# Kernel optimization log

Measured on AMD Instinct MI355X. Metric: run time of the kernel, lower is better.

The kernel has to match this reference:

```python
import jax, jax.numpy as jnp
import numpy as np

B, C_IN, H, W = 8, 64, 224, 224
C_OUT, HID = 64, 64
KH = KW = 3
IN_SZ = C_IN * KH * KW  # 576, unfold feature size (c, kh, kw order)


def setup_inputs() -> dict:
    key = jax.random.key(0)
    k_x, k_w1, k_b1, k_w2, k_b2 = jax.random.split(key, 5)
    bound1 = 1.0 / np.sqrt(IN_SZ)
    bound2 = 1.0 / np.sqrt(HID)
    return {
        "x": jax.random.normal(k_x, (B, C_IN, H, W), dtype=jnp.float32),
        "W1": jax.random.uniform(k_w1, (HID, IN_SZ), jnp.float32, -bound1, bound1),
        "b1": jax.random.uniform(k_b1, (HID,), jnp.float32, -bound1, bound1),
        "W2": jax.random.uniform(k_w2, (C_OUT, HID), jnp.float32, -bound2, bound2),
        "b2": jax.random.uniform(k_b2, (C_OUT,), jnp.float32, -bound2, bound2),
    }


def reference(x, W1, b1, W2, b2):
    # First Linear over unfold patches == implicit-GEMM conv: W1 rows are
    # flattened (c, kh, kw) exactly matching F.unfold's feature ordering.
    w_conv = W1.reshape(HID, C_IN, KH, KW)
    h = jax.lax.conv_general_dilated(
        x, w_conv,
        window_strides=(1, 1),
        padding=((1, 1), (1, 1)),
        rhs_dilation=(1, 1),
        dimension_numbers=("NCHW", "OIHW", "NCHW"),
    ) + b1[None, :, None, None]
    h = jax.nn.relu(h)
    # Second Linear acts per patch location == pointwise (1x1) contraction.
    out = jnp.einsum("bchw,oc->bohw", h, W2) + b2[None, :, None, None]
    return out
```

## Files before the change

### kernel.cpp

```cpp
#include <hip/hip_runtime.h>

typedef __attribute__((ext_vector_type(8))) short bf16x8;
typedef __attribute__((ext_vector_type(4))) float f32x4;

static constexpr int HH = 224, WW = 224;
static constexpr int CIN = 64;
static constexpr int HW = HH * WW;

__device__ __forceinline__ ushort f2bf(float f) {
    unsigned u = __builtin_bit_cast(unsigned, f);
    u += 0x7FFFu + ((u >> 16) & 1u);
    return (ushort)(u >> 16);
}

__global__ void prep_kernel(const float* __restrict__ W1, const float* __restrict__ W2,
                            ushort* __restrict__ ws, int nfill) {
    const int idx = blockIdx.x * 256 + threadIdx.x;
    if (idx < 36864) {
        const int ch = idx >> 12;
        const int n = (idx >> 6) & 63;
        const int c = idx & 63;
        ws[idx] = f2bf(W1[n * 576 + c * 9 + ch]);
    } else if (idx < 40960) {
        ws[idx] = f2bf(W2[idx - 36864]);
    } else if (idx < nfill) {
        ws[idx] = 0;
    }
}

__global__ __launch_bounds__(256)
void xprep_kernel(const float* __restrict__ xin, ushort* __restrict__ xt) {
    const int b = blockIdx.y;
    const float* xg = xin + (size_t)b * (CIN * HW);
    ushort* xo = xt + (size_t)b * ((size_t)HW * 64);
    const int base = blockIdx.x * 1024 + threadIdx.x;
    #pragma unroll
    for (int it = 0; it < 4; ++it) {
        const int idx = base + it * 256;
        const int p = ((idx >> 9) << 6) | (idx & 63);
        const int cg = (idx >> 6) & 7;
        bf16x8 o;
        #pragma unroll
        for (int j = 0; j < 8; ++j)
            o[j] = (short)f2bf(xg[(cg * 8 + j) * HW + p]);
        *reinterpret_cast<bf16x8*>(xo + (size_t)p * 64 + cg * 8) = o;
    }
}

#define GLD_LDS16(g, l) __builtin_amdgcn_global_load_lds(                  \
    (const __attribute__((address_space(1))) void*)(g),                    \
    (__attribute__((address_space(3))) void*)(l), 16, 0, 0)

__global__ __launch_bounds__(256, 3)
void mlpconv_fast(const ushort* __restrict__ xt, const ushort* __restrict__ w1r,
                  const float* __restrict__ b1, const ushort* __restrict__ w2r,
                  const float* __restrict__ b2, const ushort* __restrict__ zp,
                  float* __restrict__ out) {
    __shared__ ushort xs[10 * 40 * 64];

    const int tid = threadIdx.x;
    const int wave = tid >> 6;
    const int lane = tid & 63;
    const int l15 = lane & 15;
    const int quad = lane >> 4;

    const int x0 = blockIdx.x * 32;
    const int y0 = blockIdx.y * 8;
    const int b = blockIdx.z;

    const ushort* xtb = xt + (size_t)b * ((size_t)HW * 64);

    const int lpx = lane >> 3;
    const int laneoff = lpx * 64 + (((lane & 7) ^ lpx) * 8);

    for (int q = wave; q < 50; q += 4) {
        const int r = q / 5;
        const int i = q - 5 * r;
        const int gy = y0 + r - 1;
        const int gx0 = x0 - 4 + i * 8;
        const ushort* real = xtb + (long)(gy * WW + gx0) * 64 + laneoff;
        const bool ok = ((unsigned)gy < (unsigned)HH) &
                        ((unsigned)(gx0 + lpx) < (unsigned)WW);
        const ushort* src = ok ? real : zp;
        GLD_LDS16(src, &xs[(r * 40 + i * 8) * 64]);
    }

    float b1v[4];
    #pragma unroll
    for (int nt = 0; nt < 4; ++nt) b1v[nt] = b1[nt * 16 + l15];

    f32x4 acc[4][4];
    #pragma unroll
    for (int mt = 0; mt < 4; ++mt)
        #pragma unroll
        for (int nt = 0; nt < 4; ++nt)
            acc[mt][nt] = (f32x4){b1v[nt], b1v[nt], b1v[nt], b1v[nt]};

    asm volatile("s_waitcnt vmcnt(0)" ::: "memory");
    __syncthreads();

    #pragma unroll 2
    for (int ks = 0; ks < 18; ++ks) {
        const int ch = ks >> 1;
        const int s = ks & 1;
        const int dy = ch / 3, dx = ch - 3 * (ch / 3);
        const int ko = s * 32 + quad * 8;
        bf16x8 bfr[4];
        #pragma unroll
        for (int nt = 0; nt < 4; ++nt)
            bfr[nt] = *reinterpret_cast<const bf16x8*>(
                w1r + ch * 4096 + (nt * 16 + l15) * 64 + ko);
        const int kswz = ko ^ (((l15 + dx + 3) & 7) * 8);
        #pragma unroll
        for (int mt = 0; mt < 4; ++mt) {
            const int row = 2 * wave + (mt >> 1) + dy;
            const int col = (mt & 1) * 16 + l15 + dx + 3;
            const bf16x8 afr = *reinterpret_cast<const bf16x8*>(
                &xs[(row * 40 + col) * 64 + kswz]);
            #pragma unroll
            for (int nt = 0; nt < 4; ++nt)
                acc[mt][nt] = __builtin_amdgcn_mfma_f32_16x16x32_bf16(
                    afr, bfr[nt], acc[mt][nt], 0, 0, 0);
        }
    }

    __syncthreads();

    float4 b2q[4];
    #pragma unroll
    for (int it = 0; it < 4; ++it)
        b2q[it] = *reinterpret_cast<const float4*>(b2 + it * 16 + quad * 4);

    bf16x8 wa2[2][4];
    #pragma unroll
    for (int k2 = 0; k2 < 2; ++k2)
        #pragma unroll
        for (int it = 0; it < 4; ++it)
            wa2[k2][it] = *reinterpret_cast<const bf16x8*>(
                w2r + (it * 16 + l15) * 64 + k2 * 32 + quad * 8);

    ushort* myh = &xs[wave * (16 * 72)];
    float* outg = out + (size_t)b * (64 * HH * WW);

    #pragma unroll
    for (int mt = 0; mt < 4; ++mt) {
        #pragma unroll
        for (int ni = 0; ni < 4; ++ni)
            #pragma unroll
            for (int r = 0; r < 4; ++r) {
                float v = acc[mt][ni][r];
                v = v > 0.f ? v : 0.f;
                myh[(quad * 4 + r) * 72 + ni * 16 + l15] = f2bf(v);
            }
        f32x4 acc2[4];
        #pragma unroll
        for (int it = 0; it < 4; ++it)
            acc2[it] = (f32x4){b2q[it].x, b2q[it].y, b2q[it].z, b2q[it].w};
        #pragma unroll
        for (int k2 = 0; k2 < 2; ++k2) {
            const bf16x8 hb = *reinterpret_cast<const bf16x8*>(
                &myh[l15 * 72 + k2 * 32 + quad * 8]);
            #pragma unroll
            for (int it = 0; it < 4; ++it)
                acc2[it] = __builtin_amdgcn_mfma_f32_16x16x32_bf16(
                    wa2[k2][it], hb, acc2[it], 0, 0, 0);
        }
        const int gy = y0 + 2 * wave + (mt >> 1);
        const int gx = x0 + (mt & 1) * 16 + l15;
        #pragma unroll
        for (int it = 0; it < 4; ++it)
            #pragma unroll
            for (int r = 0; r < 4; ++r) {
                const int o = it * 16 + quad * 4 + r;
                outg[(o * HH + gy) * WW + gx] = acc2[it][r];
            }
    }
}

__global__ __launch_bounds__(256, 3)
void mlpconv_kernel(const float* __restrict__ xin, const ushort* __restrict__ w1r,
                    const float* __restrict__ b1, const ushort* __restrict__ w2r,
                    const float* __restrict__ b2, float* __restrict__ out) {
    __shared__ ushort xs[10 * 40 * 64];

    const int tid = threadIdx.x;
    const int wave = tid >> 6;
    const int lane = tid & 63;
    const int l15 = lane & 15;
    const int quad = lane >> 4;

    const int x0 = blockIdx.x * 32;
    const int y0 = blockIdx.y * 8;
    const int b = blockIdx.z;

    const float* xg = xin + (size_t)b * (CIN * HH * WW);

    for (int e = tid; e < 6400; e += 256) {
        const int i = e % 10;
        const int t = e / 10;
        const int c = t & 63;
        const int r = t >> 6;
        const int gy = y0 + r - 1;
        const int gx4 = x0 - 4 + i * 4;
        float4 v = make_float4(0.f, 0.f, 0.f, 0.f);
        if (((unsigned)gy < (unsigned)HH) && ((unsigned)gx4 <= 220u))
            v = *reinterpret_cast<const float4*>(xg + (c * HH + gy) * WW + gx4);
        const int p0 = r * 40 + i * 4;
        xs[(p0 + 0) * 64 + (c ^ (((p0 + 0) & 7) * 8))] = f2bf(v.x);
        xs[(p0 + 1) * 64 + (c ^ (((p0 + 1) & 7) * 8))] = f2bf(v.y);
        xs[(p0 + 2) * 64 + (c ^ (((p0 + 2) & 7) * 8))] = f2bf(v.z);
        xs[(p0 + 3) * 64 + (c ^ (((p0 + 3) & 7) * 8))] = f2bf(v.w);
    }

    float b1v[4];
    #pragma unroll
    for (int nt = 0; nt < 4; ++nt) b1v[nt] = b1[nt * 16 + l15];

    f32x4 acc[4][4];
    #pragma unroll
    for (int mt = 0; mt < 4; ++mt)
        #pragma unroll
        for (int nt = 0; nt < 4; ++nt)
            acc[mt][nt] = (f32x4){b1v[nt], b1v[nt], b1v[nt], b1v[nt]};

    __syncthreads();

    #pragma unroll 2
    for (int ks = 0; ks < 18; ++ks) {
        const int ch = ks >> 1;
        const int s = ks & 1;
        const int dy = ch / 3, dx = ch - 3 * (ch / 3);
        const int ko = s * 32 + quad * 8;
        bf16x8 bfr[4];
        #pragma unroll
        for (int nt = 0; nt < 4; ++nt)
            bfr[nt] = *reinterpret_cast<const bf16x8*>(
                w1r + ch * 4096 + (nt * 16 + l15) * 64 + ko);
        const int kswz = ko ^ (((l15 + dx + 3) & 7) * 8);
        #pragma unroll
        for (int mt = 0; mt < 4; ++mt) {
            const int row = 2 * wave + (mt >> 1) + dy;
            const int col = (mt & 1) * 16 + l15 + dx + 3;
            const bf16x8 afr = *reinterpret_cast<const bf16x8*>(
                &xs[(row * 40 + col) * 64 + kswz]);
            #pragma unroll
            for (int nt = 0; nt < 4; ++nt)
                acc[mt][nt] = __builtin_amdgcn_mfma_f32_16x16x32_bf16(
                    afr, bfr[nt], acc[mt][nt], 0, 0, 0);
        }
    }

    __syncthreads();

    float4 b2q[4];
    #pragma unroll
    for (int it = 0; it < 4; ++it)
        b2q[it] = *reinterpret_cast<const float4*>(b2 + it * 16 + quad * 4);

    bf16x8 wa2[2][4];
    #pragma unroll
    for (int k2 = 0; k2 < 2; ++k2)
        #pragma unroll
        for (int it = 0; it < 4; ++it)
            wa2[k2][it] = *reinterpret_cast<const bf16x8*>(
                w2r + (it * 16 + l15) * 64 + k2 * 32 + quad * 8);

    ushort* myh = &xs[wave * (16 * 72)];
    float* outg = out + (size_t)b * (64 * HH * WW);

    #pragma unroll
    for (int mt = 0; mt < 4; ++mt) {
        #pragma unroll
        for (int ni = 0; ni < 4; ++ni)
            #pragma unroll
            for (int r = 0; r < 4; ++r) {
                float v = acc[mt][ni][r];
                v = v > 0.f ? v : 0.f;
                myh[(quad * 4 + r) * 72 + ni * 16 + l15] = f2bf(v);
            }
        f32x4 acc2[4];
        #pragma unroll
        for (int it = 0; it < 4; ++it)
            acc2[it] = (f32x4){b2q[it].x, b2q[it].y, b2q[it].z, b2q[it].w};
        #pragma unroll
        for (int k2 = 0; k2 < 2; ++k2) {
            const bf16x8 hb = *reinterpret_cast<const bf16x8*>(
                &myh[l15 * 72 + k2 * 32 + quad * 8]);
            #pragma unroll
            for (int it = 0; it < 4; ++it)
                acc2[it] = __builtin_amdgcn_mfma_f32_16x16x32_bf16(
                    wa2[k2][it], hb, acc2[it], 0, 0, 0);
        }
        const int gy = y0 + 2 * wave + (mt >> 1);
        const int gx = x0 + (mt & 1) * 16 + l15;
        #pragma unroll
        for (int it = 0; it < 4; ++it)
            #pragma unroll
            for (int r = 0; r < 4; ++r) {
                const int o = it * 16 + quad * 4 + r;
                outg[(o * HH + gy) * WW + gx] = acc2[it][r];
            }
    }
}

extern "C" void kernel_launch(void* const* d_in, const int* in_sizes, int n_in,
                              void* d_out, int out_size, void* d_ws, size_t ws_size,
                              hipStream_t stream) {
    const float* x  = (const float*)d_in[0];
    const float* W1 = (const float*)d_in[1];
    const float* b1 = (const float*)d_in[2];
    const float* W2 = (const float*)d_in[3];
    const float* b2 = (const float*)d_in[4];
    float* out = (float*)d_out;

    ushort* ws  = (ushort*)d_ws;
    ushort* w1r = ws;
    ushort* w2r = ws + 36864;
    ushort* zp  = ws + 40960;
    ushort* xt  = ws + 41024;

    const size_t need = (size_t)41024 * 2 + (size_t)8 * HW * 64 * 2;
    const bool fast = ws_size >= need;

    prep_kernel<<<161, 256, 0, stream>>>(W1, W2, ws, fast ? 41024 : 40960);
    dim3 grid(WW / 32, HH / 8, 8);
    if (fast) {
        xprep_kernel<<<dim3(392, 8), 256, 0, stream>>>(x, xt);
        mlpconv_fast<<<grid, dim3(256), 0, stream>>>(xt, w1r, b1, w2r, b2, zp, out);
    } else {
        mlpconv_kernel<<<grid, dim3(256), 0, stream>>>(x, w1r, b1, w2r, b2, out);
    }
}
```

Baseline: 302.3 us.

## Double-buffer W1 register prefetch in conv loop and vectorize x transpose loads

The main conv loop now keeps two register buffers of W1 fragments, so the weights for the next kernel tap load while MFMAs run on the current tap. This is meant to hide global-load latency that the old loop exposed by loading weights just before use. The x prep kernel now reads float4 vectors across 4 pixels per channel and writes 4 bf16x8 outputs per thread, which widens the global loads. The cost is higher register pressure from the extra 16 bf16x8 fragments, which could hurt occupancy under launch bounds of 3.

```diff
diff --git a/kernel.cpp b/kernel.cpp
--- a/kernel.cpp
+++ b/kernel.cpp
@@ -33,23 +33,61 @@
     const int b = blockIdx.y;
     const float* xg = xin + (size_t)b * (CIN * HW);
     ushort* xo = xt + (size_t)b * ((size_t)HW * 64);
-    const int base = blockIdx.x * 1024 + threadIdx.x;
-    #pragma unroll
-    for (int it = 0; it < 4; ++it) {
-        const int idx = base + it * 256;
-        const int p = ((idx >> 9) << 6) | (idx & 63);
-        const int cg = (idx >> 6) & 7;
+    const int idx = blockIdx.x * 256 + threadIdx.x;
+    const int cg = idx & 7;
+    const int p4 = idx >> 3;
+    const float* src = xg + (size_t)(cg * 8) * HW + p4 * 4;
+    float4 v[8];
+    #pragma unroll
+    for (int j = 0; j < 8; ++j)
+        v[j] = *reinterpret_cast<const float4*>(src + (size_t)j * HW);
+    #pragma unroll
+    for (int k = 0; k < 4; ++k) {
         bf16x8 o;
         #pragma unroll
         for (int j = 0; j < 8; ++j)
-            o[j] = (short)f2bf(xg[(cg * 8 + j) * HW + p]);
-        *reinterpret_cast<bf16x8*>(xo + (size_t)p * 64 + cg * 8) = o;
+            o[j] = (short)f2bf(reinterpret_cast<const float*>(&v[j])[k]);
+        *reinterpret_cast<bf16x8*>(xo + (size_t)(p4 * 4 + k) * 64 + cg * 8) = o;
     }
 }
 
 #define GLD_LDS16(g, l) __builtin_amdgcn_global_load_lds(                  \
     (const __attribute__((address_space(1))) void*)(g),                    \
     (__attribute__((address_space(3))) void*)(l), 16, 0, 0)
+
+__device__ __forceinline__ void loadw_r(bf16x8 (&buf)[2][4],
+                                        const ushort* __restrict__ w1r,
+                                        int ch, int l15, int quad) {
+    #pragma unroll
+    for (int s = 0; s < 2; ++s)
+        #pragma unroll
+        for (int nt = 0; nt < 4; ++nt)
+            buf[s][nt] = *reinterpret_cast<const bf16x8*>(
+                w1r + ch * 4096 + (nt * 16 + l15) * 64 + s * 32 + quad * 8);
+}
+
+__device__ __forceinline__ void step_r(const bf16x8 (&buf)[2][4],
+                                       f32x4 (&acc)[4][4],
+                                       const ushort* xs,
+                                       int ch, int wave, int l15, int quad) {
+    const int dy = ch / 3, dx = ch - 3 * (ch / 3);
+    #pragma unroll
+    for (int s = 0; s < 2; ++s) {
+        const int ko = s * 32 + quad * 8;
+        const int kswz = ko ^ (((l15 + dx + 3) & 7) * 8);
+        #pragma unroll
+        for (int mt = 0; mt < 4; ++mt) {
+            const int row = 2 * wave + (mt >> 1) + dy;
+            const int col = (mt & 1) * 16 + l15 + dx + 3;
+            const bf16x8 afr = *reinterpret_cast<const bf16x8*>(
+                &xs[(row * 40 + col) * 64 + kswz]);
+            #pragma unroll
+            for (int nt = 0; nt < 4; ++nt)
+                acc[mt][nt] = __builtin_amdgcn_mfma_f32_16x16x32_bf16(
+                    afr, buf[s][nt], acc[mt][nt], 0, 0, 0);
+        }
+    }
+}
 
 __global__ __launch_bounds__(256, 3)
 void mlpconv_fast(const ushort* __restrict__ xt, const ushort* __restrict__ w1r,
@@ -96,33 +134,24 @@
         for (int nt = 0; nt < 4; ++nt)
             acc[mt][nt] = (f32x4){b1v[nt], b1v[nt], b1v[nt], b1v[nt]};
 
+    bf16x8 bA[2][4], bB[2][4];
+    loadw_r(bA, w1r, 0, l15, quad);
+    loadw_r(bB, w1r, 1, l15, quad);
+
     asm volatile("s_waitcnt vmcnt(0)" ::: "memory");
     __syncthreads();
 
-    #pragma unroll 2
-    for (int ks = 0; ks < 18; ++ks) {
-        const int ch = ks >> 1;
-        const int s = ks & 1;
-        const int dy = ch / 3, dx = ch - 3 * (ch / 3);
-        const int ko = s * 32 + quad * 8;
-        bf16x8 bfr[4];
-        #pragma unroll
-        for (int nt = 0; nt < 4; ++nt)
-            bfr[nt] = *reinterpret_cast<const bf16x8*>(
-                w1r + ch * 4096 + (nt * 16 + l15) * 64 + ko);
-        const int kswz = ko ^ (((l15 + dx + 3) & 7) * 8);
-        #pragma unroll
-        for (int mt = 0; mt < 4; ++mt) {
-            const int row = 2 * wave + (mt >> 1) + dy;
-            const int col = (mt & 1) * 16 + l15 + dx + 3;
-            const bf16x8 afr = *reinterpret_cast<const bf16x8*>(
-                &xs[(row * 40 + col) * 64 + kswz]);
-            #pragma unroll
-            for (int nt = 0; nt < 4; ++nt)
-                acc[mt][nt] = __builtin_amdgcn_mfma_f32_16x16x32_bf16(
-                    afr, bfr[nt], acc[mt][nt], 0, 0, 0);
-        }
-    }
+    #pragma unroll 1
+    for (int cp = 0; cp < 3; ++cp) {
+        step_r(bA, acc, xs, 2 * cp,     wave, l15, quad);
+        loadw_r(bA, w1r, 2 * cp + 2, l15, quad);
+        step_r(bB, acc, xs, 2 * cp + 1, wave, l15, quad);
+        loadw_r(bB, w1r, 2 * cp + 3, l15, quad);
+    }
+    step_r(bA, acc, xs, 6, wave, l15, quad);
+    loadw_r(bA, w1r, 8, l15, quad);
+    step_r(bB, acc, xs, 7, wave, l15, quad);
+    step_r(bA, acc, xs, 8, wave, l15, quad);
 
     __syncthreads();
 
```

New measurement: 300.5 us. Within noise of the previous version (-0.6%).
